# Optimization experiments

Measured on AMD Instinct MI355X. Metric: run time of the kernel, lower is better.

## Reference

```python
import jax, jax.numpy as jnp
import numpy as np

N = 100000   # n_nodes
E = 1600000  # n_edges (avg degree 16)
IN, HID, OUT = 128, 128, 64


def setup_inputs() -> dict:
    key = jax.random.key(0)
    k0, k1, k2, k3 = jax.random.split(key, 4)
    x = jax.random.normal(k0, (N, IN), dtype=jnp.float32)
    edge_index = jax.random.randint(k1, (2, E), 0, N, dtype=jnp.int32)
    # Glorot-ish init for GCNConv weights, zero bias (PyG default bias=True)
    W1 = jax.random.normal(k2, (IN, HID), dtype=jnp.float32) * (1.0 / np.sqrt(IN))
    b1 = jnp.zeros((HID,), dtype=jnp.float32)
    W2 = jax.random.normal(k3, (HID, OUT), dtype=jnp.float32) * (1.0 / np.sqrt(HID))
    b2 = jnp.zeros((OUT,), dtype=jnp.float32)
    return {"x": x, "W1": W1, "b1": b1, "W2": W2, "b2": b2, "edge_index": edge_index}


def gcn_layer(x, W, b, src, dst):
    """PyG GCNConv: add self-loops, symmetric deg^{-1/2} normalization,
    linear transform, scatter-add aggregation at dst, plus bias."""
    n = x.shape[0]
    h = x @ W                                   # [n, d_out]
    loops = jnp.arange(n, dtype=src.dtype)
    s = jnp.concatenate([src, loops])           # sources incl. self-loops
    d = jnp.concatenate([dst, loops])           # targets incl. self-loops
    deg = jax.ops.segment_sum(jnp.ones_like(d, dtype=h.dtype), d, num_segments=n)
    dinv = jnp.where(deg > 0, jax.lax.rsqrt(deg), 0.0)
    norm = dinv[s] * dinv[d]                    # [E+n]
    msg = h[s] * norm[:, None]                  # gather + scale
    out = jax.ops.segment_sum(msg, d, num_segments=n)  # scatter-add
    return out + b


def reference(x, W1, b1, W2, b2, edge_index):
    src, dst = edge_index[0], edge_index[1]
    h = jax.nn.relu(gcn_layer(x, W1, b1, src, dst))
    return gcn_layer(h, W2, b2, src, dst)
```

## Files before the change

kernel.cpp:

```cpp
#include <hip/hip_runtime.h>

#define NNODES 100000
#define NEDGES 1600000
#define IND 128
#define HIDD 128
#define OUTD 64

#define BSHIFT 9
#define BSIZE  512
#define NBUCK  ((NNODES + BSIZE - 1) / BSIZE)
#define SLACK  9216
#define BIN_EPB  8192
#define SEG_CAP  10240

typedef unsigned int  uint32;
typedef __attribute__((ext_vector_type(8))) short short8;
typedef __attribute__((ext_vector_type(4))) float floatx4;

__device__ __forceinline__ unsigned short f2bf(float f) {
    union { float f; uint32 u; } x; x.f = f;
    uint32 u = x.u;
    return (unsigned short)((u + 0x7fffu + ((u >> 16) & 1u)) >> 16);
}
__device__ __forceinline__ float bflo(uint32 u) {
    union { uint32 i; float f; } x; x.i = u << 16; return x.f;
}
__device__ __forceinline__ float bfhi(uint32 u) {
    union { uint32 i; float f; } x; x.i = u & 0xffff0000u; return x.f;
}

__global__ void k_bin(const int* __restrict__ src, const int* __restrict__ dst,
                      int* __restrict__ bcnt, uint32* __restrict__ staging, int e) {
    __shared__ int lh[NBUCK];
    __shared__ int lcur[NBUCK];
    const int tid = threadIdx.x;
    for (int i = tid; i < NBUCK; i += 256) lh[i] = 0;
    __syncthreads();

    int start = blockIdx.x * BIN_EPB;
    int end = min(start + BIN_EPB, e);

    for (int i = start + tid; i < end; i += 256)
        atomicAdd(&lh[dst[i] >> BSHIFT], 1);
    __syncthreads();

    for (int i = tid; i < NBUCK; i += 256)
        lcur[i] = lh[i] ? atomicAdd(&bcnt[i], lh[i]) : 0;
    __syncthreads();

    for (int i = start + tid; i < end; i += 256) {
        int d = dst[i], s = src[i];
        int b = d >> BSHIFT;
        int pos = atomicAdd(&lcur[b], 1);
        if (pos < SLACK)
            staging[b * SLACK + pos] = ((uint32)(d & (BSIZE - 1)) << 17) | (uint32)s;
    }
}

__global__ void k_bscan(const int* __restrict__ bcnt, int* __restrict__ boff) {
    __shared__ int buf[256];
    const int tid = threadIdx.x;
    int v = (tid < NBUCK) ? bcnt[tid] : 0;
    buf[tid] = v;
    __syncthreads();
    for (int off = 1; off < 256; off <<= 1) {
        int t = (tid >= off) ? buf[tid - off] : 0;
        __syncthreads();
        buf[tid] += t;
        __syncthreads();
    }
    if (tid < NBUCK) boff[tid] = buf[tid] - v;
    if (tid == 255) boff[NBUCK] = buf[255];
}

__global__ void k_fill3(const uint32* __restrict__ staging, const int* __restrict__ bcnt,
                        const int* __restrict__ boff,
                        int* __restrict__ row_ptr, int* __restrict__ csr_src,
                        float* __restrict__ dinv, int n) {
    __shared__ int nc[BSIZE];
    __shared__ int lcur[BSIZE];
    __shared__ int sbuf[256];
    __shared__ int seg[SEG_CAP];
    const int b = blockIdx.x;
    const int base = b << BSHIFT;
    const int tid = threadIdx.x;
    const int nn = min(BSIZE, n - base);

    for (int i = tid; i < BSIZE; i += 256) nc[i] = 0;
    __syncthreads();

    const uint32* st = staging + (size_t)b * SLACK;
    const int cnt = bcnt[b];
    for (int i = tid; i < cnt; i += 256)
        atomicAdd(&nc[st[i] >> 17], 1);
    __syncthreads();

    int a0 = nc[2 * tid], a1 = nc[2 * tid + 1];
    sbuf[tid] = a0 + a1;
    __syncthreads();
    for (int off = 1; off < 256; off <<= 1) {
        int t = (tid >= off) ? sbuf[tid - off] : 0;
        __syncthreads();
        sbuf[tid] += t;
        __syncthreads();
    }
    int ex = sbuf[tid] - (a0 + a1);
    const int r0 = boff[b];
    if (2 * tid < nn) {
        row_ptr[base + 2 * tid] = r0 + ex;
        dinv[base + 2 * tid] = rsqrtf((float)(a0 + 1));
    }
    if (2 * tid + 1 < nn) {
        row_ptr[base + 2 * tid + 1] = r0 + ex + a0;
        dinv[base + 2 * tid + 1] = rsqrtf((float)(a1 + 1));
    }
    lcur[2 * tid] = ex;
    lcur[2 * tid + 1] = ex + a0;
    if (b == (int)gridDim.x - 1 && tid == 255) row_ptr[n] = boff[NBUCK];
    __syncthreads();

    for (int i = tid; i < cnt; i += 256) {
        uint32 p = st[i];
        int dl = (int)(p >> 17);
        int s  = (int)(p & 0x1FFFFu);
        int pos = atomicAdd(&lcur[dl], 1);
        if (pos < SEG_CAP) seg[pos] = s;
        else               csr_src[r0 + pos] = s;
    }
    __syncthreads();
    int lim = min(cnt, SEG_CAP);
    for (int i = tid; i < lim; i += 256) csr_src[r0 + i] = seg[i];
}

__global__ void k_wt_both(const float* __restrict__ W1, const float* __restrict__ W2,
                          unsigned short* __restrict__ wt1, unsigned short* __restrict__ wt2) {
    int idx = blockIdx.x * 256 + threadIdx.x;
    if (idx < IND * HIDD) {
        int k = idx / HIDD, m = idx - k * HIDD;
        wt1[m * IND + k] = f2bf(W1[idx]);
    } else {
        int j = idx - IND * HIDD;
        if (j < HIDD * OUTD) {
            int k = j / OUTD, m = j - k * OUTD;
            wt2[m * HIDD + k] = f2bf(W2[j]);
        }
    }
}

template<int K, int M, bool ABF16>
__launch_bounds__(256)
__global__ void gemm_mfma(const void* __restrict__ Ap, const unsigned short* __restrict__ WT,
                          const float* __restrict__ dinv, unsigned short* __restrict__ C, int n) {
    constexpr int KP = K + 8;
    constexpr int NT = M / 16;
    __shared__ unsigned short Asl[64 * KP];
    __shared__ unsigned short Wsl[M * KP];

    const int tid = threadIdx.x;
    const int row0 = blockIdx.x * 64;

    {
        constexpr int SEG = (K * 2) / 16;
        const uint4* srcp = (const uint4*)WT;
        for (int idx = tid; idx < M * SEG; idx += 256) {
            int r = idx / SEG, s = idx - r * SEG;
            *(uint4*)(Wsl + r * KP + s * 8) = srcp[idx];
        }
    }
    if constexpr (ABF16) {
        constexpr int U4R = K / 8;
        const unsigned short* Ab = (const unsigned short*)Ap;
        for (int idx = tid; idx < 64 * U4R; idx += 256) {
            int r = idx / U4R, s = idx - r * U4R;
            int grow = row0 + r; if (grow >= n) grow = n - 1;
            *(uint4*)(Asl + r * KP + s * 8) = *(const uint4*)(Ab + (size_t)grow * K + s * 8);
        }
    } else {
        constexpr int F4R = K / 4;
        const float* Af = (const float*)Ap;
        for (int idx = tid; idx < 64 * F4R; idx += 256) {
            int r = idx / F4R, s = idx - r * F4R;
            int grow = row0 + r; if (grow >= n) grow = n - 1;
            float4 v = *(const float4*)(Af + (size_t)grow * K + s * 4);
            uint32 p0 = (uint32)f2bf(v.x) | ((uint32)f2bf(v.y) << 16);
            uint32 p1 = (uint32)f2bf(v.z) | ((uint32)f2bf(v.w) << 16);
            *(uint2*)(Asl + r * KP + s * 4) = make_uint2(p0, p1);
        }
    }
    __syncthreads();

    const int lane = tid & 63;
    const int wave = tid >> 6;
    const int mm = lane & 15;
    const int qq = lane >> 4;

    floatx4 acc[NT];
#pragma unroll
    for (int t = 0; t < NT; t++) acc[t] = (floatx4){0.f, 0.f, 0.f, 0.f};

#pragma unroll
    for (int kc = 0; kc < K / 32; kc++) {
        short8 a = *(const short8*)(Asl + (wave * 16 + mm) * KP + kc * 32 + qq * 8);
#pragma unroll
        for (int t = 0; t < NT; t++) {
            short8 b = *(const short8*)(Wsl + (t * 16 + mm) * KP + kc * 32 + qq * 8);
            acc[t] = __builtin_amdgcn_mfma_f32_16x16x32_bf16(a, b, acc[t], 0, 0, 0);
        }
    }

#pragma unroll
    for (int r = 0; r < 4; r++) {
        int grow = row0 + wave * 16 + qq * 4 + r;
        if (grow < n) {
            float dv = dinv[grow];
#pragma unroll
            for (int t = 0; t < NT; t++)
                C[(size_t)grow * M + t * 16 + mm] = f2bf(acc[t][r] * dv);
        }
    }
}

template<int M, bool RELU, bool OBF16>
__launch_bounds__(256)
__global__ void gather_k(const unsigned short* __restrict__ h,
                         const int* __restrict__ row_ptr,
                         const int* __restrict__ csr_src,
                         const float* __restrict__ dinv,
                         const float* __restrict__ bias,
                         void* __restrict__ outp, int n) {
    constexpr int LPG = M / 8;
    constexpr int GPB = 256 / LPG;
    const int g = threadIdx.x / LPG;
    const int l = threadIdx.x % LPG;
    const int v = blockIdx.x * GPB + g;
    if (v >= n) return;

    const float dv = dinv[v];
    float acc[8];
    {
        uint4 u = *(const uint4*)(h + (size_t)v * M + l * 8);
        acc[0] = bflo(u.x); acc[1] = bfhi(u.x);
        acc[2] = bflo(u.y); acc[3] = bfhi(u.y);
        acc[4] = bflo(u.z); acc[5] = bfhi(u.z);
        acc[6] = bflo(u.w); acc[7] = bfhi(u.w);
    }

    int j   = row_ptr[v];
    int end = row_ptr[v + 1];
    for (; j + 3 < end; j += 4) {
        int s0 = csr_src[j];
        int s1 = csr_src[j + 1];
        int s2 = csr_src[j + 2];
        int s3 = csr_src[j + 3];
        uint4 u0 = *(const uint4*)(h + (size_t)s0 * M + l * 8);
        uint4 u1 = *(const uint4*)(h + (size_t)s1 * M + l * 8);
        uint4 u2 = *(const uint4*)(h + (size_t)s2 * M + l * 8);
        uint4 u3 = *(const uint4*)(h + (size_t)s3 * M + l * 8);
        acc[0] += (bflo(u0.x) + bflo(u1.x)) + (bflo(u2.x) + bflo(u3.x));
        acc[1] += (bfhi(u0.x) + bfhi(u1.x)) + (bfhi(u2.x) + bfhi(u3.x));
        acc[2] += (bflo(u0.y) + bflo(u1.y)) + (bflo(u2.y) + bflo(u3.y));
        acc[3] += (bfhi(u0.y) + bfhi(u1.y)) + (bfhi(u2.y) + bfhi(u3.y));
        acc[4] += (bflo(u0.z) + bflo(u1.z)) + (bflo(u2.z) + bflo(u3.z));
        acc[5] += (bfhi(u0.z) + bfhi(u1.z)) + (bfhi(u2.z) + bfhi(u3.z));
        acc[6] += (bflo(u0.w) + bflo(u1.w)) + (bflo(u2.w) + bflo(u3.w));
        acc[7] += (bfhi(u0.w) + bfhi(u1.w)) + (bfhi(u2.w) + bfhi(u3.w));
    }
    for (; j < end; j++) {
        int s0 = csr_src[j];
        uint4 u0 = *(const uint4*)(h + (size_t)s0 * M + l * 8);
        acc[0] += bflo(u0.x); acc[1] += bfhi(u0.x);
        acc[2] += bflo(u0.y); acc[3] += bfhi(u0.y);
        acc[4] += bflo(u0.z); acc[5] += bfhi(u0.z);
        acc[6] += bflo(u0.w); acc[7] += bfhi(u0.w);
    }

#pragma unroll
    for (int i = 0; i < 8; i++) {
        acc[i] = acc[i] * dv + bias[l * 8 + i];
        if (RELU) acc[i] = fmaxf(acc[i], 0.0f);
    }

    if constexpr (OBF16) {
        uint32 p[4];
#pragma unroll
        for (int c = 0; c < 4; c++)
            p[c] = (uint32)f2bf(acc[2 * c]) | ((uint32)f2bf(acc[2 * c + 1]) << 16);
        *(uint4*)((unsigned short*)outp + (size_t)v * M + l * 8) = make_uint4(p[0], p[1], p[2], p[3]);
    } else {
        float* op = (float*)outp + (size_t)v * M + l * 8;
        *(float4*)op = make_float4(acc[0], acc[1], acc[2], acc[3]);
        *(float4*)(op + 4) = make_float4(acc[4], acc[5], acc[6], acc[7]);
    }
}

extern "C" void kernel_launch(void* const* d_in, const int* in_sizes, int n_in,
                              void* d_out, int out_size, void* d_ws, size_t ws_size,
                              hipStream_t stream) {
    const float* x  = (const float*)d_in[0];
    const float* W1 = (const float*)d_in[1];
    const float* b1 = (const float*)d_in[2];
    const float* W2 = (const float*)d_in[3];
    const float* b2 = (const float*)d_in[4];
    const int*   ei = (const int*)d_in[5];
    const int* src = ei;
    const int* dst = ei + NEDGES;
    float* out = (float*)d_out;

    char* ws = (char*)d_ws;
    float*  dinv    = (float*)ws;   ws += (size_t)NNODES * 4;
    int*    row_ptr = (int*)ws;     ws += (size_t)(NNODES + 4) * 4;
    int*    bcnt    = (int*)ws;     ws += 256 * 4;
    int*    boff    = (int*)ws;     ws += 260 * 4;
    unsigned short* wt1 = (unsigned short*)ws;  ws += (size_t)IND * HIDD * 2;
    unsigned short* wt2 = (unsigned short*)ws;  ws += (size_t)HIDD * OUTD * 2;
    int*    csr_src = (int*)ws;     ws += (size_t)NEDGES * 4;
    uint32* staging = (uint32*)ws;  ws += (size_t)NBUCK * SLACK * 4;
    unsigned short* hr  = (unsigned short*)ws;  ws += (size_t)NNODES * HIDD * 2;
    unsigned short* hbf = (unsigned short*)ws;

    hipMemsetAsync(bcnt, 0, 256 * 4, stream);
    k_bin<<<(NEDGES + BIN_EPB - 1) / BIN_EPB, 256, 0, stream>>>(src, dst, bcnt, staging, NEDGES);
    k_bscan<<<1, 256, 0, stream>>>(bcnt, boff);
    k_fill3<<<NBUCK, 256, 0, stream>>>(staging, bcnt, boff, row_ptr, csr_src, dinv, NNODES);

    k_wt_both<<<(IND * HIDD + HIDD * OUTD + 255) / 256, 256, 0, stream>>>(W1, W2, wt1, wt2);

    gemm_mfma<IND, HIDD, false><<<(NNODES + 63) / 64, 256, 0, stream>>>(
        x, wt1, dinv, hbf, NNODES);
    gather_k<HIDD, true, true><<<(NNODES * (HIDD / 8) + 255) / 256, 256, 0, stream>>>(
        hbf, row_ptr, csr_src, dinv, b1, hr, NNODES);

    gemm_mfma<HIDD, OUTD, true><<<(NNODES + 63) / 64, 256, 0, stream>>>(
        hr, wt2, dinv, hbf, NNODES);
    gather_k<OUTD, false, false><<<(NNODES * (OUTD / 8) + 255) / 256, 256, 0, stream>>>(
        hbf, row_ptr, csr_src, dinv, b2, out, NNODES);
}
```

Baseline: 321.0 us.

## Store hidden features in 16-column chunks and pin chunks to XCDs for gather

The GEMMs now write their bf16 outputs in a chunked layout: 16-feature column slabs, each holding all nodes. The gather kernels are restructured so that every block handles one slab, picked from blockIdx modulo 8, which under round-robin dispatch maps each slab to a single XCD. Each XCD's L2 then only has to cache a 3.2MB slab instead of the whole feature matrix. Edge index loads and output stores also become nontemporal. In exchange, every node's edge list is re-read once per slab, and the code assumes round-robin block-to-XCD placement.

```diff
diff --git a/kernel.cpp b/kernel.cpp
--- a/kernel.cpp
+++ b/kernel.cpp
@@ -13,9 +13,13 @@
 #define BIN_EPB  8192
 #define SEG_CAP  10240
 
+#define HALFN 50000
+
 typedef unsigned int  uint32;
 typedef __attribute__((ext_vector_type(8))) short short8;
 typedef __attribute__((ext_vector_type(4))) float floatx4;
+typedef __attribute__((ext_vector_type(4))) unsigned int uivec4;
+typedef __attribute__((ext_vector_type(4))) float fvec4;
 
 __device__ __forceinline__ unsigned short f2bf(float f) {
     union { float f; uint32 u; } x; x.f = f;
@@ -173,7 +177,8 @@
         for (int idx = tid; idx < 64 * U4R; idx += 256) {
             int r = idx / U4R, s = idx - r * U4R;
             int grow = row0 + r; if (grow >= n) grow = n - 1;
-            *(uint4*)(Asl + r * KP + s * 8) = *(const uint4*)(Ab + (size_t)grow * K + s * 8);
+            *(uint4*)(Asl + r * KP + s * 8) =
+                *(const uint4*)(Ab + ((size_t)(s >> 1) * n + grow) * 16 + (s & 1) * 8);
         }
     } else {
         constexpr int F4R = K / 4;
@@ -212,33 +217,46 @@
     for (int r = 0; r < 4; r++) {
         int grow = row0 + wave * 16 + qq * 4 + r;
         if (grow < n) {
-            float dv = dinv[grow];
+            float dvv = dinv[grow];
 #pragma unroll
             for (int t = 0; t < NT; t++)
-                C[(size_t)grow * M + t * 16 + mm] = f2bf(acc[t][r] * dv);
-        }
-    }
-}
-
-template<int M, bool RELU, bool OBF16>
+                C[((size_t)t * n + grow) * 16 + mm] = f2bf(acc[t][r] * dvv);
+        }
+    }
+}
+
+template<int CH, bool RELU, bool OBF16>
 __launch_bounds__(256)
-__global__ void gather_k(const unsigned short* __restrict__ h,
+__global__ void gather_c(const unsigned short* __restrict__ h,
                          const int* __restrict__ row_ptr,
                          const int* __restrict__ csr_src,
                          const float* __restrict__ dinv,
                          const float* __restrict__ bias,
                          void* __restrict__ outp, int n) {
-    constexpr int LPG = M / 8;
-    constexpr int GPB = 256 / LPG;
-    const int g = threadIdx.x / LPG;
-    const int l = threadIdx.x % LPG;
-    const int v = blockIdx.x * GPB + g;
-    if (v >= n) return;
-
+    const int bid = blockIdx.x;
+    const int xcd = bid & 7;
+    int chunk, v0, vend;
+    if constexpr (CH == 8) {
+        chunk = xcd;
+        v0 = (bid >> 3) * 128;
+        vend = n;
+    } else {
+        chunk = xcd & 3;
+        const int sub = xcd >> 2;
+        v0 = sub * HALFN + (bid >> 3) * 128;
+        vend = min(n, sub * HALFN + HALFN);
+    }
+    const int g  = threadIdx.x >> 1;
+    const int l8 = (threadIdx.x & 1) * 8;
+    const int v = v0 + g;
+    if (v >= vend) return;
+
+    const unsigned short* __restrict__ hc = h + (size_t)chunk * n * 16;
     const float dv = dinv[v];
+
     float acc[8];
     {
-        uint4 u = *(const uint4*)(h + (size_t)v * M + l * 8);
+        uint4 u = *(const uint4*)(hc + (size_t)v * 16 + l8);
         acc[0] = bflo(u.x); acc[1] = bfhi(u.x);
         acc[2] = bflo(u.y); acc[3] = bfhi(u.y);
         acc[4] = bflo(u.z); acc[5] = bfhi(u.z);
@@ -246,16 +264,16 @@
     }
 
     int j   = row_ptr[v];
-    int end = row_ptr[v + 1];
+    const int end = row_ptr[v + 1];
     for (; j + 3 < end; j += 4) {
-        int s0 = csr_src[j];
-        int s1 = csr_src[j + 1];
-        int s2 = csr_src[j + 2];
-        int s3 = csr_src[j + 3];
-        uint4 u0 = *(const uint4*)(h + (size_t)s0 * M + l * 8);
-        uint4 u1 = *(const uint4*)(h + (size_t)s1 * M + l * 8);
-        uint4 u2 = *(const uint4*)(h + (size_t)s2 * M + l * 8);
-        uint4 u3 = *(const uint4*)(h + (size_t)s3 * M + l * 8);
+        int s0 = __builtin_nontemporal_load(csr_src + j);
+        int s1 = __builtin_nontemporal_load(csr_src + j + 1);
+        int s2 = __builtin_nontemporal_load(csr_src + j + 2);
+        int s3 = __builtin_nontemporal_load(csr_src + j + 3);
+        uint4 u0 = *(const uint4*)(hc + (size_t)s0 * 16 + l8);
+        uint4 u1 = *(const uint4*)(hc + (size_t)s1 * 16 + l8);
+        uint4 u2 = *(const uint4*)(hc + (size_t)s2 * 16 + l8);
+        uint4 u3 = *(const uint4*)(hc + (size_t)s3 * 16 + l8);
         acc[0] += (bflo(u0.x) + bflo(u1.x)) + (bflo(u2.x) + bflo(u3.x));
         acc[1] += (bfhi(u0.x) + bfhi(u1.x)) + (bfhi(u2.x) + bfhi(u3.x));
         acc[2] += (bflo(u0.y) + bflo(u1.y)) + (bflo(u2.y) + bflo(u3.y));
@@ -266,8 +284,8 @@
         acc[7] += (bfhi(u0.w) + bfhi(u1.w)) + (bfhi(u2.w) + bfhi(u3.w));
     }
     for (; j < end; j++) {
-        int s0 = csr_src[j];
-        uint4 u0 = *(const uint4*)(h + (size_t)s0 * M + l * 8);
+        int s0 = __builtin_nontemporal_load(csr_src + j);
+        uint4 u0 = *(const uint4*)(hc + (size_t)s0 * 16 + l8);
         acc[0] += bflo(u0.x); acc[1] += bfhi(u0.x);
         acc[2] += bflo(u0.y); acc[3] += bfhi(u0.y);
         acc[4] += bflo(u0.z); acc[5] += bfhi(u0.z);
@@ -276,20 +294,23 @@
 
 #pragma unroll
     for (int i = 0; i < 8; i++) {
-        acc[i] = acc[i] * dv + bias[l * 8 + i];
+        acc[i] = acc[i] * dv + bias[chunk * 16 + l8 + i];
         if (RELU) acc[i] = fmaxf(acc[i], 0.0f);
     }
 
     if constexpr (OBF16) {
-        uint32 p[4];
+        uivec4 p;
 #pragma unroll
         for (int c = 0; c < 4; c++)
             p[c] = (uint32)f2bf(acc[2 * c]) | ((uint32)f2bf(acc[2 * c + 1]) << 16);
-        *(uint4*)((unsigned short*)outp + (size_t)v * M + l * 8) = make_uint4(p[0], p[1], p[2], p[3]);
+        __builtin_nontemporal_store(p,
+            (uivec4*)((unsigned short*)outp + ((size_t)chunk * n + v) * 16 + l8));
     } else {
-        float* op = (float*)outp + (size_t)v * M + l * 8;
-        *(float4*)op = make_float4(acc[0], acc[1], acc[2], acc[3]);
-        *(float4*)(op + 4) = make_float4(acc[4], acc[5], acc[6], acc[7]);
+        float* op = (float*)outp + (size_t)v * OUTD + chunk * 16 + l8;
+        fvec4 a0 = {acc[0], acc[1], acc[2], acc[3]};
+        fvec4 a1 = {acc[4], acc[5], acc[6], acc[7]};
+        __builtin_nontemporal_store(a0, (fvec4*)op);
+        __builtin_nontemporal_store(a1, (fvec4*)(op + 4));
     }
 }
 
@@ -325,13 +346,16 @@
 
     k_wt_both<<<(IND * HIDD + HIDD * OUTD + 255) / 256, 256, 0, stream>>>(W1, W2, wt1, wt2);
 
+    const int NB1 = (NNODES + 127) / 128;
+    const int NB2 = (HALFN  + 127) / 128;
+
     gemm_mfma<IND, HIDD, false><<<(NNODES + 63) / 64, 256, 0, stream>>>(
         x, wt1, dinv, hbf, NNODES);
-    gather_k<HIDD, true, true><<<(NNODES * (HIDD / 8) + 255) / 256, 256, 0, stream>>>(
+    gather_c<8, true, true><<<8 * NB1, 256, 0, stream>>>(
         hbf, row_ptr, csr_src, dinv, b1, hr, NNODES);
 
     gemm_mfma<HIDD, OUTD, true><<<(NNODES + 63) / 64, 256, 0, stream>>>(
         hr, wt2, dinv, hbf, NNODES);
-    gather_k<OUTD, false, false><<<(NNODES * (OUTD / 8) + 255) / 256, 256, 0, stream>>>(
+    gather_c<4, false, false><<<8 * NB2, 256, 0, stream>>>(
         hbf, row_ptr, csr_src, dinv, b2, out, NNODES);
 }
```

Result: slower. 391.0 us (+21.8%).

## Fold bucket scan and weight transpose into neighbor kernels; nontemporal gather loads/stores

Applied to the files above, without the earlier changes.

Removes two small kernel launches: the weight bf16 transpose runs as extra blocks of the binning kernel, and each fill block redoes the 196-bucket prefix scan in shared memory instead of relying on a separate scan kernel. The gather kernels now use nontemporal loads for CSR indices and nontemporal stores for outputs so that streaming data does not displace the gathered feature rows from cache. The cost is a redundant scan in every fill block and more shared memory per block, and the nontemporal hints may interact with caching in ways that are hard to predict.

```diff
diff --git a/kernel.cpp b/kernel.cpp
--- a/kernel.cpp
+++ b/kernel.cpp
@@ -12,10 +12,14 @@
 #define SLACK  9216
 #define BIN_EPB  8192
 #define SEG_CAP  10240
+#define BINB   ((NEDGES + BIN_EPB - 1) / BIN_EPB)
+#define WTB    ((IND * HIDD + HIDD * OUTD + 255) / 256)
 
 typedef unsigned int  uint32;
 typedef __attribute__((ext_vector_type(8))) short short8;
 typedef __attribute__((ext_vector_type(4))) float floatx4;
+typedef __attribute__((ext_vector_type(4))) unsigned int uivec4;
+typedef __attribute__((ext_vector_type(4))) float fvec4;
 
 __device__ __forceinline__ unsigned short f2bf(float f) {
     union { float f; uint32 u; } x; x.f = f;
@@ -30,10 +34,27 @@
 }
 
 __global__ void k_bin(const int* __restrict__ src, const int* __restrict__ dst,
-                      int* __restrict__ bcnt, uint32* __restrict__ staging, int e) {
+                      int* __restrict__ bcnt, uint32* __restrict__ staging, int e,
+                      const float* __restrict__ W1, const float* __restrict__ W2,
+                      unsigned short* __restrict__ wt1, unsigned short* __restrict__ wt2) {
+    const int tid = threadIdx.x;
+    if (blockIdx.x >= BINB) {
+        int idx = (blockIdx.x - BINB) * 256 + tid;
+        if (idx < IND * HIDD) {
+            int k = idx / HIDD, m = idx - k * HIDD;
+            wt1[m * IND + k] = f2bf(W1[idx]);
+        } else {
+            int j = idx - IND * HIDD;
+            if (j < HIDD * OUTD) {
+                int k = j / OUTD, m = j - k * OUTD;
+                wt2[m * HIDD + k] = f2bf(W2[j]);
+            }
+        }
+        return;
+    }
+
     __shared__ int lh[NBUCK];
     __shared__ int lcur[NBUCK];
-    const int tid = threadIdx.x;
     for (int i = tid; i < NBUCK; i += 256) lh[i] = 0;
     __syncthreads();
 
@@ -57,29 +78,13 @@
     }
 }
 
-__global__ void k_bscan(const int* __restrict__ bcnt, int* __restrict__ boff) {
-    __shared__ int buf[256];
-    const int tid = threadIdx.x;
-    int v = (tid < NBUCK) ? bcnt[tid] : 0;
-    buf[tid] = v;
-    __syncthreads();
-    for (int off = 1; off < 256; off <<= 1) {
-        int t = (tid >= off) ? buf[tid - off] : 0;
-        __syncthreads();
-        buf[tid] += t;
-        __syncthreads();
-    }
-    if (tid < NBUCK) boff[tid] = buf[tid] - v;
-    if (tid == 255) boff[NBUCK] = buf[255];
-}
-
 __global__ void k_fill3(const uint32* __restrict__ staging, const int* __restrict__ bcnt,
-                        const int* __restrict__ boff,
                         int* __restrict__ row_ptr, int* __restrict__ csr_src,
                         float* __restrict__ dinv, int n) {
     __shared__ int nc[BSIZE];
     __shared__ int lcur[BSIZE];
     __shared__ int sbuf[256];
+    __shared__ int boffl[NBUCK + 1];
     __shared__ int seg[SEG_CAP];
     const int b = blockIdx.x;
     const int base = b << BSHIFT;
@@ -87,16 +92,9 @@
     const int nn = min(BSIZE, n - base);
 
     for (int i = tid; i < BSIZE; i += 256) nc[i] = 0;
-    __syncthreads();
-
-    const uint32* st = staging + (size_t)b * SLACK;
-    const int cnt = bcnt[b];
-    for (int i = tid; i < cnt; i += 256)
-        atomicAdd(&nc[st[i] >> 17], 1);
-    __syncthreads();
-
-    int a0 = nc[2 * tid], a1 = nc[2 * tid + 1];
-    sbuf[tid] = a0 + a1;
+
+    int vb = (tid < NBUCK) ? bcnt[tid] : 0;
+    sbuf[tid] = vb;
     __syncthreads();
     for (int off = 1; off < 256; off <<= 1) {
         int t = (tid >= off) ? sbuf[tid - off] : 0;
@@ -104,8 +102,27 @@
         sbuf[tid] += t;
         __syncthreads();
     }
+    if (tid < NBUCK) boffl[tid] = sbuf[tid] - vb;
+    if (tid == 255) boffl[NBUCK] = sbuf[255];
+    __syncthreads();
+
+    const uint32* st = staging + (size_t)b * SLACK;
+    const int cnt = bcnt[b];
+    for (int i = tid; i < cnt; i += 256)
+        atomicAdd(&nc[st[i] >> 17], 1);
+    __syncthreads();
+
+    int a0 = nc[2 * tid], a1 = nc[2 * tid + 1];
+    sbuf[tid] = a0 + a1;
+    __syncthreads();
+    for (int off = 1; off < 256; off <<= 1) {
+        int t = (tid >= off) ? sbuf[tid - off] : 0;
+        __syncthreads();
+        sbuf[tid] += t;
+        __syncthreads();
+    }
     int ex = sbuf[tid] - (a0 + a1);
-    const int r0 = boff[b];
+    const int r0 = boffl[b];
     if (2 * tid < nn) {
         row_ptr[base + 2 * tid] = r0 + ex;
         dinv[base + 2 * tid] = rsqrtf((float)(a0 + 1));
@@ -116,7 +133,7 @@
     }
     lcur[2 * tid] = ex;
     lcur[2 * tid + 1] = ex + a0;
-    if (b == (int)gridDim.x - 1 && tid == 255) row_ptr[n] = boff[NBUCK];
+    if (b == (int)gridDim.x - 1 && tid == 255) row_ptr[n] = boffl[NBUCK];
     __syncthreads();
 
     for (int i = tid; i < cnt; i += 256) {
@@ -130,21 +147,6 @@
     __syncthreads();
     int lim = min(cnt, SEG_CAP);
     for (int i = tid; i < lim; i += 256) csr_src[r0 + i] = seg[i];
-}
-
-__global__ void k_wt_both(const float* __restrict__ W1, const float* __restrict__ W2,
-                          unsigned short* __restrict__ wt1, unsigned short* __restrict__ wt2) {
-    int idx = blockIdx.x * 256 + threadIdx.x;
-    if (idx < IND * HIDD) {
-        int k = idx / HIDD, m = idx - k * HIDD;
-        wt1[m * IND + k] = f2bf(W1[idx]);
-    } else {
-        int j = idx - IND * HIDD;
-        if (j < HIDD * OUTD) {
-            int k = j / OUTD, m = j - k * OUTD;
-            wt2[m * HIDD + k] = f2bf(W2[j]);
-        }
-    }
 }
 
 template<int K, int M, bool ABF16>
@@ -248,10 +250,10 @@
     int j   = row_ptr[v];
     int end = row_ptr[v + 1];
     for (; j + 3 < end; j += 4) {
-        int s0 = csr_src[j];
-        int s1 = csr_src[j + 1];
-        int s2 = csr_src[j + 2];
-        int s3 = csr_src[j + 3];
+        int s0 = __builtin_nontemporal_load(csr_src + j);
+        int s1 = __builtin_nontemporal_load(csr_src + j + 1);
+        int s2 = __builtin_nontemporal_load(csr_src + j + 2);
+        int s3 = __builtin_nontemporal_load(csr_src + j + 3);
         uint4 u0 = *(const uint4*)(h + (size_t)s0 * M + l * 8);
         uint4 u1 = *(const uint4*)(h + (size_t)s1 * M + l * 8);
         uint4 u2 = *(const uint4*)(h + (size_t)s2 * M + l * 8);
@@ -266,7 +268,7 @@
         acc[7] += (bfhi(u0.w) + bfhi(u1.w)) + (bfhi(u2.w) + bfhi(u3.w));
     }
     for (; j < end; j++) {
-        int s0 = csr_src[j];
+        int s0 = __builtin_nontemporal_load(csr_src + j);
         uint4 u0 = *(const uint4*)(h + (size_t)s0 * M + l * 8);
         acc[0] += bflo(u0.x); acc[1] += bfhi(u0.x);
         acc[2] += bflo(u0.y); acc[3] += bfhi(u0.y);
@@ -281,15 +283,18 @@
     }
 
     if constexpr (OBF16) {
-        uint32 p[4];
+        uivec4 p;
 #pragma unroll
         for (int c = 0; c < 4; c++)
             p[c] = (uint32)f2bf(acc[2 * c]) | ((uint32)f2bf(acc[2 * c + 1]) << 16);
-        *(uint4*)((unsigned short*)outp + (size_t)v * M + l * 8) = make_uint4(p[0], p[1], p[2], p[3]);
+        __builtin_nontemporal_store(p,
+            (uivec4*)((unsigned short*)outp + (size_t)v * M + l * 8));
     } else {
         float* op = (float*)outp + (size_t)v * M + l * 8;
-        *(float4*)op = make_float4(acc[0], acc[1], acc[2], acc[3]);
-        *(float4*)(op + 4) = make_float4(acc[4], acc[5], acc[6], acc[7]);
+        fvec4 a0 = {acc[0], acc[1], acc[2], acc[3]};
+        fvec4 a1 = {acc[4], acc[5], acc[6], acc[7]};
+        __builtin_nontemporal_store(a0, (fvec4*)op);
+        __builtin_nontemporal_store(a1, (fvec4*)(op + 4));
     }
 }
 
@@ -319,11 +324,8 @@
     unsigned short* hbf = (unsigned short*)ws;
 
     hipMemsetAsync(bcnt, 0, 256 * 4, stream);
-    k_bin<<<(NEDGES + BIN_EPB - 1) / BIN_EPB, 256, 0, stream>>>(src, dst, bcnt, staging, NEDGES);
-    k_bscan<<<1, 256, 0, stream>>>(bcnt, boff);
-    k_fill3<<<NBUCK, 256, 0, stream>>>(staging, bcnt, boff, row_ptr, csr_src, dinv, NNODES);
-
-    k_wt_both<<<(IND * HIDD + HIDD * OUTD + 255) / 256, 256, 0, stream>>>(W1, W2, wt1, wt2);
+    k_bin<<<BINB + WTB, 256, 0, stream>>>(src, dst, bcnt, staging, NEDGES, W1, W2, wt1, wt2);
+    k_fill3<<<NBUCK, 256, 0, stream>>>(staging, bcnt, row_ptr, csr_src, dinv, NNODES);
 
     gemm_mfma<IND, HIDD, false><<<(NNODES + 63) / 64, 256, 0, stream>>>(
         x, wt1, dinv, hbf, NNODES);
```

After: 326.7 us. Within noise of the previous version (+1.8%).
